# Kernel optimization log

Measured on AMD Instinct MI355X. Metric: run time of the kernel, lower is better.

The kernel has to match this reference:

```python
import jax, jax.numpy as jnp
import numpy as np

B, T, E = 4, 2048, 2048
H, KV = 16, 4
G = H // KV           # GQA group size
D = E // H            # head_dim = 128


def setup_inputs() -> dict:
    key = jax.random.key(0)
    kx, kq, kk, kv, ko = jax.random.split(key, 5)
    s = 1.0 / np.sqrt(E).astype(np.float32)
    x  = jax.random.normal(kx, (B, T, E), jnp.float32)
    Wq = jax.random.normal(kq, (E, H * D), jnp.float32) * s
    Wk = jax.random.normal(kk, (E, KV * D), jnp.float32) * s
    Wv = jax.random.normal(kv, (E, KV * D), jnp.float32) * s
    Wo = jax.random.normal(ko, (H * D, E), jnp.float32) * s
    return {"x": x, "Wq": Wq, "Wk": Wk, "Wv": Wv, "Wo": Wo}


def reference(x, Wq, Wk, Wv, Wo):
    # causal=True (default in the torch module)
    b, t, _ = x.shape
    scale = 1.0 / np.sqrt(D).astype(np.float32)
    # q heads ordered so that reshape (H,)->(KV,G) matches torch repeat_interleave
    q = (x @ Wq).reshape(b, t, KV, G, D)   # (B,T,KV,G,D)
    k = (x @ Wk).reshape(b, t, KV, D)      # (B,T,KV,D)
    v = (x @ Wv).reshape(b, t, KV, D)
    # scores per (kv-head h, group member g): (B,KV,G,T,T)
    scores = jnp.einsum('bqhgd,bkhd->bhgqk', q, k) * scale
    causal_mask = jnp.tril(jnp.ones((t, t), dtype=bool))  # True = keep
    scores = jnp.where(causal_mask, scores, -jnp.inf)
    w = jax.nn.softmax(scores, axis=-1)
    y = jnp.einsum('bhgqk,bkhd->bqhgd', w, v)  # (B,T,KV,G,D)
    y = y.reshape(b, t, H * D)
    return y @ Wo
```

## Files before the change

kernel.cpp:

```cpp
#include <hip/hip_runtime.h>

typedef unsigned short u16;
typedef __attribute__((ext_vector_type(8))) __bf16 bf16x8;
typedef __attribute__((ext_vector_type(4))) float f32x4;

#define BB 4
#define TT 2048
#define EE 2048
#define HH 16
#define KVH 4
#define DD 128

static __device__ __forceinline__ u16 f2bf(float f) {
  unsigned int u = __float_as_uint(f);
  u += 0x7fffu + ((u >> 16) & 1u);
  return (u16)(u >> 16);
}

static __device__ __forceinline__ void gl_lds16(const u16* g, u16* l) {
  __builtin_amdgcn_global_load_lds((__attribute__((address_space(1))) void*)g,
                                   (__attribute__((address_space(3))) void*)l,
                                   16, 0, 0);
}

__global__ __launch_bounds__(256) void cvt_f32_bf16(const float* __restrict__ in,
                                                    u16* __restrict__ out, int n4) {
  int i = blockIdx.x * 256 + threadIdx.x;
  if (i >= n4) return;
  float4 v = ((const float4*)in)[i];
  union { uint2 u2; u16 s[4]; } o;
  o.s[0] = f2bf(v.x); o.s[1] = f2bf(v.y); o.s[2] = f2bf(v.z); o.s[3] = f2bf(v.w);
  ((uint2*)out)[i] = o.u2;
}

__global__ __launch_bounds__(256) void transpose_w(const float* __restrict__ W,
                                                   u16* __restrict__ Wt, int R, int C) {
  __shared__ float tile[32][33];
  int tx = threadIdx.x & 31, ty = threadIdx.x >> 5;
  int r0 = blockIdx.y * 32, c0 = blockIdx.x * 32;
  #pragma unroll
  for (int i = ty; i < 32; i += 8)
    tile[i][tx] = W[(size_t)(r0 + i) * C + (c0 + tx)];
  __syncthreads();
  #pragma unroll
  for (int i = ty; i < 32; i += 8)
    Wt[(size_t)(c0 + i) * R + (r0 + tx)] = f2bf(tile[tx][i]);
}

__global__ __launch_bounds__(256) void transpose_v(const u16* __restrict__ KVb,
                                                   u16* __restrict__ VTg) {
  __shared__ u16 tile[32][36];
  const int tid = threadIdx.x;
  const int t0 = blockIdx.x * 32, d0 = blockIdx.y * 32;
  const int z = blockIdx.z;
  const int vb = z * 128;
  const size_t srcbase = (size_t)(z >> 2) * TT * 1024 + 512 + (z & 3) * 128;
  {
    int i = tid >> 3, c4 = (tid & 7) * 4;
    union { uint2 u; u16 s[4]; } r;
    r.u = *(const uint2*)(KVb + srcbase + (size_t)(t0 + i) * 1024 + d0 + c4);
    tile[i][c4] = r.s[0]; tile[i][c4 + 1] = r.s[1];
    tile[i][c4 + 2] = r.s[2]; tile[i][c4 + 3] = r.s[3];
  }
  __syncthreads();
  {
    int j = tid >> 3, cc = (tid & 7) * 4;
    union { uint2 u; u16 s[4]; } w;
    w.s[0] = tile[cc][j]; w.s[1] = tile[cc + 1][j];
    w.s[2] = tile[cc + 2][j]; w.s[3] = tile[cc + 3][j];
    *(uint2*)(VTg + (size_t)(vb + d0 + j) * TT + t0 + cc) = w.u;
  }
}

template <int MODE>
__global__ __launch_bounds__(512) void gemm256(const u16* __restrict__ A,
                                               const u16* __restrict__ Bt0,
                                               const u16* __restrict__ Bt1,
                                               void* __restrict__ C0,
                                               void* __restrict__ C1,
                                               int M, int N0, int N1, int K, int nbx) {
  __shared__ __align__(16) u16 sh[2][4][8192];
  const int tid = threadIdx.x;
  const int lane = tid & 63, wave = tid >> 6;
  const int quad = lane >> 4, n16 = lane & 15;
  const int mi = wave >> 2, ni = wave & 3;

  const int nwg = gridDim.x;
  int wg = blockIdx.x;
  wg = (wg & 7) * (nwg >> 3) + (wg >> 3);
  const int bx = wg % nbx, by = wg / nbx;
  const size_t rowbase = (size_t)by * 256;
  const int colbase = bx * 256;

  const u16* Bt = Bt0;
  int bcol = colbase;
  if (MODE == 1 && colbase >= N0) { Bt = Bt1; bcol = colbase - N0; }

  const int c0 = tid, c1 = tid + 512;
  const int r0s = c0 >> 3, ci0 = (c0 & 7) ^ (r0s & 7);
  const int r1s = c1 >> 3, ci1 = (c1 & 7) ^ (r1s & 7);
  const u16* Ag0 = A + (rowbase + r0s) * (size_t)K + ci0 * 8;
  const u16* Ag1 = A + (rowbase + r1s) * (size_t)K + ci1 * 8;
  const u16* Bg0 = Bt + ((size_t)bcol + r0s) * K + ci0 * 8;
  const u16* Bg1 = Bt + ((size_t)bcol + r1s) * K + ci1 * 8;
  const size_t h128K = (size_t)128 * K;

#define STAGE(ob, h, kb) do {                                              \
    if ((h) < 2) {                                                         \
      gl_lds16(Ag0 + (size_t)(h) * h128K + (kb), &sh[ob][h][c0 * 8]);      \
      gl_lds16(Ag1 + (size_t)(h) * h128K + (kb), &sh[ob][h][c1 * 8]);      \
    } else {                                                               \
      gl_lds16(Bg0 + (size_t)((h) - 2) * h128K + (kb), &sh[ob][h][c0 * 8]);\
      gl_lds16(Bg1 + (size_t)((h) - 2) * h128K + (kb), &sh[ob][h][c1 * 8]);\
    } } while (0)

#define LDA_HALF(mh) do {                                                  \
    _Pragma("unroll") for (int m = 0; m < 4; ++m)                          \
      _Pragma("unroll") for (int kk = 0; kk < 2; ++kk) {                   \
        int row_ = ((mh) * 4 + m) * 16 + n16;                              \
        int c_ = row_ * 8 + ((kk * 4 + quad) ^ (n16 & 7));                 \
        af[m][kk] = *(const bf16x8*)&sh[buf][mi][c_ * 8];                  \
      } } while (0)

#define LDB_HALF(nh, BF) do {                                              \
    _Pragma("unroll") for (int n = 0; n < 2; ++n)                          \
      _Pragma("unroll") for (int kk = 0; kk < 2; ++kk) {                   \
        int row_ = (ni & 1) * 64 + ((nh) * 2 + n) * 16 + n16;              \
        int c_ = row_ * 8 + ((kk * 4 + quad) ^ (n16 & 7));                 \
        BF[n][kk] = *(const bf16x8*)&sh[buf][2 + (ni >> 1)][c_ * 8];       \
      } } while (0)

#define DO_QUAD(mh, nh, BF) do {                                           \
    __builtin_amdgcn_s_setprio(1);                                         \
    _Pragma("unroll") for (int m = 0; m < 4; ++m)                          \
      _Pragma("unroll") for (int n = 0; n < 2; ++n)                        \
        _Pragma("unroll") for (int kk = 0; kk < 2; ++kk)                   \
          acc[(mh) * 4 + m][(nh) * 2 + n] =                                \
              __builtin_amdgcn_mfma_f32_16x16x32_bf16(                     \
                  af[m][kk], BF[n][kk], acc[(mh) * 4 + m][(nh) * 2 + n],   \
                  0, 0, 0);                                                \
    __builtin_amdgcn_s_setprio(0);                                         \
  } while (0)

#define FENCE() asm volatile("" ::: "memory")

  f32x4 acc[8][4];
  #pragma unroll
  for (int i = 0; i < 8; ++i)
    #pragma unroll
    for (int j = 0; j < 4; ++j) acc[i][j] = (f32x4){0.f, 0.f, 0.f, 0.f};

  bf16x8 af[4][2], bf0[2][2], bf1[2][2];
  const int nt = K / 64;

  STAGE(0, 0, 0); STAGE(0, 1, 0); STAGE(0, 2, 0); STAGE(0, 3, 0);

  #pragma unroll 2
  for (int t = 0; t < nt; ++t) {
    const int buf = t & 1, ob = buf ^ 1;
    const int kbn = (t + 1) * 64;
    const bool pre = (t + 1 < nt);

    if (pre) {
      STAGE(ob, 0, kbn);
      asm volatile("s_waitcnt vmcnt(2)" ::: "memory");
    } else {
      asm volatile("s_waitcnt vmcnt(0)" ::: "memory");
    }
    __builtin_amdgcn_s_barrier(); FENCE();
    LDA_HALF(0); LDB_HALF(0, bf0);
    DO_QUAD(0, 0, bf0);
    __builtin_amdgcn_s_barrier(); FENCE();

    LDB_HALF(1, bf1);
    if (pre) STAGE(ob, 1, kbn);
    __builtin_amdgcn_s_barrier(); FENCE();
    DO_QUAD(0, 1, bf1);
    __builtin_amdgcn_s_barrier(); FENCE();

    LDA_HALF(1);
    if (pre) STAGE(ob, 2, kbn);
    __builtin_amdgcn_s_barrier(); FENCE();
    DO_QUAD(1, 1, bf1);
    __builtin_amdgcn_s_barrier(); FENCE();

    if (pre) STAGE(ob, 3, kbn);
    __builtin_amdgcn_s_barrier(); FENCE();
    DO_QUAD(1, 0, bf0);
    __builtin_amdgcn_s_barrier(); FENCE();
  }

#undef STAGE
#undef LDA_HALF
#undef LDB_HALF
#undef DO_QUAD
#undef FENCE

  const size_t crow0 = rowbase + (size_t)mi * 128;
  #pragma unroll
  for (int mt = 0; mt < 8; ++mt) {
    #pragma unroll
    for (int r = 0; r < 4; ++r) {
      size_t row = crow0 + mt * 16 + quad * 4 + r;
      #pragma unroll
      for (int nt_ = 0; nt_ < 4; ++nt_) {
        int col = colbase + ni * 64 + nt_ * 16 + n16;
        float v = acc[mt][nt_][r];
        if (MODE == 0) {
          ((float*)C0)[row * (size_t)N0 + col] = v;
        } else {
          if (col < N0) ((u16*)C0)[row * (size_t)N0 + col] = f2bf(v);
          else          ((u16*)C1)[row * (size_t)N1 + (col - N0)] = f2bf(v);
        }
      }
    }
  }
}

__global__ __launch_bounds__(256) void attn_kernel(const u16* __restrict__ Qm,
                                                   const u16* __restrict__ KVm,
                                                   const u16* __restrict__ VTg,
                                                   u16* __restrict__ Ym) {
  __shared__ u16 Ks[32 * 128];
  __shared__ u16 Vt[128 * 32];
  __shared__ u16 Pb[4 * 32 * 40];

  const int tid = threadIdx.x;
  const int lane = tid & 63, wave = tid >> 6;
  const int quad = lane >> 4, n16 = lane & 15;
  const int b = blockIdx.y >> 4, h = blockIdx.y & 15;
  const int kvh = h >> 2;
  const int kvbase = b * TT;
  const u16* VTg_ = VTg + (size_t)((b * 4 + kvh) * 128) * TT;

  const int krow = tid >> 4;
  const int kslot = tid & 15;
  const int kg = (kslot ^ krow) * 8;
  u16* Ksd0 = &Ks[krow * 128 + kslot * 8];
  u16* Ksd1 = &Ks[(krow + 16) * 128 + kslot * 8];
  const int vrow = tid >> 2, vc = (tid & 3) * 8;
  u16* Vtd0 = &Vt[vrow * 32 + vc];
  u16* Vtd1 = &Vt[(vrow + 64) * 32 + vc];

  constexpr float SCL = 0.08838834764831843f * 1.4426950408889634f;

  for (int pass = 0; pass < 2; ++pass) {
    const int qt = pass ? 15 - (int)blockIdx.x : (int)blockIdx.x;
    const int q0 = qt * 128;
    const size_t qrowbase = (size_t)(b * TT + q0);
    const int wq0 = wave * 32;

    bf16x8 aq[2][4];
    #pragma unroll
    for (int mt = 0; mt < 2; ++mt) {
      const u16* qp = Qm + (qrowbase + wq0 + mt * 16 + n16) * (HH * DD) + h * DD + quad * 8;
      #pragma unroll
      for (int dt = 0; dt < 4; ++dt)
        aq[mt][dt] = *(const bf16x8*)(qp + dt * 32);
    }

    float lrow[2][4];
    f32x4 oacc[2][8];
    #pragma unroll
    for (int mt = 0; mt < 2; ++mt) {
      #pragma unroll
      for (int r = 0; r < 4; ++r) lrow[mt][r] = 0.f;
      #pragma unroll
      for (int i = 0; i < 8; ++i) oacc[mt][i] = (f32x4){0.f, 0.f, 0.f, 0.f};
    }

    const int kend = q0 + 128;
    for (int kb = 0; kb < kend; kb += 32) {
      __syncthreads();
      gl_lds16(KVm + (size_t)(kvbase + kb + krow) * 1024 + kvh * DD + kg, Ksd0);
      gl_lds16(KVm + (size_t)(kvbase + kb + krow + 16) * 1024 + kvh * DD + kg, Ksd1);
      gl_lds16(VTg_ + (size_t)vrow * TT + kb + vc, Vtd0);
      gl_lds16(VTg_ + (size_t)(vrow + 64) * TT + kb + vc, Vtd1);
      __syncthreads();

      f32x4 sf[2][2];
      #pragma unroll
      for (int half = 0; half < 2; ++half) {
        bf16x8 bk[4];
        #pragma unroll
        for (int dt = 0; dt < 4; ++dt) {
          int slot = (dt * 4 + quad) ^ n16;
          bk[dt] = *(const bf16x8*)&Ks[(half * 16 + n16) * 128 + slot * 8];
        }
        #pragma unroll
        for (int mt = 0; mt < 2; ++mt) {
          f32x4 s = (f32x4){0.f, 0.f, 0.f, 0.f};
          #pragma unroll
          for (int dt = 0; dt < 4; ++dt)
            s = __builtin_amdgcn_mfma_f32_16x16x32_bf16(aq[mt][dt], bk[dt], s, 0, 0, 0);
          sf[mt][half] = s;
        }
      }

      u16* pw = &Pb[wave * (32 * 40)];
      #pragma unroll
      for (int mt = 0; mt < 2; ++mt)
        #pragma unroll
        for (int half = 0; half < 2; ++half) {
          int key = kb + half * 16 + n16;
          #pragma unroll
          for (int r = 0; r < 4; ++r) {
            int qpos = q0 + wq0 + mt * 16 + quad * 4 + r;
            float pv = (key <= qpos) ? exp2f(sf[mt][half][r] * SCL) : 0.f;
            lrow[mt][r] += pv;
            pw[(mt * 16 + quad * 4 + r) * 40 + half * 16 + n16] = f2bf(pv);
          }
        }
      __builtin_amdgcn_s_waitcnt(0);
      bf16x8 ap[2];
      ap[0] = *(const bf16x8*)&pw[n16 * 40 + quad * 8];
      ap[1] = *(const bf16x8*)&pw[(16 + n16) * 40 + quad * 8];

      #pragma unroll
      for (int dt = 0; dt < 8; ++dt) {
        bf16x8 bv = *(const bf16x8*)&Vt[(dt * 16 + n16) * 32 + quad * 8];
        oacc[0][dt] = __builtin_amdgcn_mfma_f32_16x16x32_bf16(ap[0], bv, oacc[0][dt], 0, 0, 0);
        oacc[1][dt] = __builtin_amdgcn_mfma_f32_16x16x32_bf16(ap[1], bv, oacc[1][dt], 0, 0, 0);
      }
    }

    float rinv[2][4];
    #pragma unroll
    for (int mt = 0; mt < 2; ++mt)
      #pragma unroll
      for (int r = 0; r < 4; ++r) {
        float v = lrow[mt][r];
        v += __shfl_xor(v, 1, 64);
        v += __shfl_xor(v, 2, 64);
        v += __shfl_xor(v, 4, 64);
        v += __shfl_xor(v, 8, 64);
        rinv[mt][r] = 1.0f / v;
      }
    #pragma unroll
    for (int mt = 0; mt < 2; ++mt)
      #pragma unroll
      for (int dt = 0; dt < 8; ++dt)
        #pragma unroll
        for (int r = 0; r < 4; ++r) {
          size_t row = qrowbase + wq0 + mt * 16 + quad * 4 + r;
          Ym[row * (HH * DD) + h * DD + dt * 16 + n16] = f2bf(oacc[mt][dt][r] * rinv[mt][r]);
        }
  }
}

extern "C" void kernel_launch(void* const* d_in, const int* in_sizes, int n_in,
                              void* d_out, int out_size, void* d_ws, size_t ws_size,
                              hipStream_t stream) {
  const float* x  = (const float*)d_in[0];
  const float* Wq = (const float*)d_in[1];
  const float* Wk = (const float*)d_in[2];
  const float* Wv = (const float*)d_in[3];
  const float* Wo = (const float*)d_in[4];
  float* out = (float*)d_out;

  u16* ws   = (u16*)d_ws;
  u16* xb   = ws;
  u16* Wbuf = xb + (size_t)8192 * 2048;
  u16* Yb   = xb;

  u16* ob   = (u16*)d_out;
  u16* Qb   = ob;
  u16* KVb  = ob + (size_t)8192 * 2048;
  u16* VTg  = ob + (size_t)8192 * 2048 + (size_t)8192 * 1024;
  u16* WkvT = VTg + (size_t)16 * 128 * 2048;

  cvt_f32_bf16<<<16384, 256, 0, stream>>>(x, xb, (4 * 2048 * 2048) / 4);

  transpose_w<<<dim3(64, 64), 256, 0, stream>>>(Wq, Wbuf, 2048, 2048);
  transpose_w<<<dim3(16, 64), 256, 0, stream>>>(Wk, WkvT, 2048, 512);
  transpose_w<<<dim3(16, 64), 256, 0, stream>>>(Wv, WkvT + (size_t)512 * 2048, 2048, 512);

  gemm256<1><<<384, 512, 0, stream>>>(xb, Wbuf, WkvT, (void*)Qb, (void*)KVb,
                                      8192, 2048, 1024, 2048, 12);

  transpose_v<<<dim3(64, 4, 16), 256, 0, stream>>>(KVb, VTg);

  attn_kernel<<<dim3(8, 64), 256, 0, stream>>>(Qb, KVb, VTg, Yb);

  transpose_w<<<dim3(64, 64), 256, 0, stream>>>(Wo, Wbuf, 2048, 2048);
  gemm256<0><<<256, 512, 0, stream>>>(Yb, Wbuf, nullptr, (void*)out, nullptr,
                                      8192, 2048, 0, 2048, 8);
}
```

Measured before the change: 477.4 us.

## Double-buffer K/V staging in attention, one q-tile per block, skip masked tiles

The attention kernel now double-buffers its K and V tiles in LDS, prefetching the next key block with async global-to-LDS loads while the current one is computed, and waits on the vmcnt counter instead of a pair of __syncthreads. The two-pass work balancing (pairing tile i with 15-i) is replaced by a grid of 16 q-tiles with the heaviest tiles first. Waves skip key blocks that lie fully beyond their causal window, apply the mask only on diagonal blocks, pack probabilities with v_cvt_pk_bf16_f32, swizzle the V tile layout against bank conflicts, and raise wave priority around MFMA sections. This trades more LDS per block and a less even per-block workload for overlap of loads with compute and less masking and conversion work.

```diff
diff --git a/kernel.cpp b/kernel.cpp
--- a/kernel.cpp
+++ b/kernel.cpp
@@ -221,8 +221,8 @@
                                                    const u16* __restrict__ KVm,
                                                    const u16* __restrict__ VTg,
                                                    u16* __restrict__ Ym) {
-  __shared__ u16 Ks[32 * 128];
-  __shared__ u16 Vt[128 * 32];
+  __shared__ u16 Ks[2][32 * 128];
+  __shared__ u16 Vt[2][128 * 32];
   __shared__ u16 Pb[4 * 32 * 40];
 
   const int tid = threadIdx.x;
@@ -233,51 +233,63 @@
   const int kvbase = b * TT;
   const u16* VTg_ = VTg + (size_t)((b * 4 + kvh) * 128) * TT;
 
-  const int krow = tid >> 4;
-  const int kslot = tid & 15;
+  const int krow = tid >> 4, kslot = tid & 15;
   const int kg = (kslot ^ krow) * 8;
-  u16* Ksd0 = &Ks[krow * 128 + kslot * 8];
-  u16* Ksd1 = &Ks[(krow + 16) * 128 + kslot * 8];
-  const int vrow = tid >> 2, vc = (tid & 3) * 8;
-  u16* Vtd0 = &Vt[vrow * 32 + vc];
-  u16* Vtd1 = &Vt[(vrow + 64) * 32 + vc];
+  const int vrow = tid >> 2, vs = tid & 3;
+  const int vq8 = (vs ^ ((tid >> 3) & 3)) * 8;
+
+#define STAGEKV(bi, kb) do {                                                          \
+    gl_lds16(KVm + (size_t)(kvbase + (kb) + krow) * 1024 + kvh * DD + kg,             \
+             &Ks[bi][krow * 128 + kslot * 8]);                                        \
+    gl_lds16(KVm + (size_t)(kvbase + (kb) + krow + 16) * 1024 + kvh * DD + kg,        \
+             &Ks[bi][(krow + 16) * 128 + kslot * 8]);                                 \
+    gl_lds16(VTg_ + (size_t)vrow * TT + (kb) + vq8, &Vt[bi][vrow * 32 + vs * 8]);     \
+    gl_lds16(VTg_ + (size_t)(vrow + 64) * TT + (kb) + vq8,                            \
+             &Vt[bi][(vrow + 64) * 32 + vs * 8]);                                     \
+  } while (0)
 
   constexpr float SCL = 0.08838834764831843f * 1.4426950408889634f;
 
-  for (int pass = 0; pass < 2; ++pass) {
-    const int qt = pass ? 15 - (int)blockIdx.x : (int)blockIdx.x;
-    const int q0 = qt * 128;
-    const size_t qrowbase = (size_t)(b * TT + q0);
-    const int wq0 = wave * 32;
-
-    bf16x8 aq[2][4];
-    #pragma unroll
-    for (int mt = 0; mt < 2; ++mt) {
-      const u16* qp = Qm + (qrowbase + wq0 + mt * 16 + n16) * (HH * DD) + h * DD + quad * 8;
-      #pragma unroll
-      for (int dt = 0; dt < 4; ++dt)
-        aq[mt][dt] = *(const bf16x8*)(qp + dt * 32);
+  const int qt = 15 - (int)blockIdx.x;
+  const int q0 = qt * 128;
+  const size_t qrowbase = (size_t)(b * TT + q0);
+  const int wq0 = wave * 32;
+  const int qmin = q0 + wq0;
+
+  bf16x8 aq[2][4];
+  #pragma unroll
+  for (int mt = 0; mt < 2; ++mt) {
+    const u16* qp = Qm + (qrowbase + wq0 + mt * 16 + n16) * (HH * DD) + h * DD + quad * 8;
+    #pragma unroll
+    for (int dt = 0; dt < 4; ++dt)
+      aq[mt][dt] = *(const bf16x8*)(qp + dt * 32);
+  }
+
+  float lrow[2][4];
+  f32x4 oacc[2][8];
+  #pragma unroll
+  for (int mt = 0; mt < 2; ++mt) {
+    #pragma unroll
+    for (int r = 0; r < 4; ++r) lrow[mt][r] = 0.f;
+    #pragma unroll
+    for (int i = 0; i < 8; ++i) oacc[mt][i] = (f32x4){0.f, 0.f, 0.f, 0.f};
+  }
+
+  const int kend = q0 + 128;
+  STAGEKV(0, 0);
+  for (int kb = 0; kb < kend; kb += 32) {
+    const int bi = (kb >> 5) & 1;
+    const bool pre = (kb + 32 < kend);
+    if (pre) {
+      STAGEKV(bi ^ 1, kb + 32);
+      asm volatile("s_waitcnt vmcnt(4)" ::: "memory");
+    } else {
+      asm volatile("s_waitcnt vmcnt(0)" ::: "memory");
     }
-
-    float lrow[2][4];
-    f32x4 oacc[2][8];
-    #pragma unroll
-    for (int mt = 0; mt < 2; ++mt) {
-      #pragma unroll
-      for (int r = 0; r < 4; ++r) lrow[mt][r] = 0.f;
-      #pragma unroll
-      for (int i = 0; i < 8; ++i) oacc[mt][i] = (f32x4){0.f, 0.f, 0.f, 0.f};
-    }
-
-    const int kend = q0 + 128;
-    for (int kb = 0; kb < kend; kb += 32) {
-      __syncthreads();
-      gl_lds16(KVm + (size_t)(kvbase + kb + krow) * 1024 + kvh * DD + kg, Ksd0);
-      gl_lds16(KVm + (size_t)(kvbase + kb + krow + 16) * 1024 + kvh * DD + kg, Ksd1);
-      gl_lds16(VTg_ + (size_t)vrow * TT + kb + vc, Vtd0);
-      gl_lds16(VTg_ + (size_t)(vrow + 64) * TT + kb + vc, Vtd1);
-      __syncthreads();
-
+    __builtin_amdgcn_s_barrier();
+    asm volatile("" ::: "memory");
+
+    if (kb <= qmin + 31) {
       f32x4 sf[2][2];
       #pragma unroll
       for (int half = 0; half < 2; ++half) {
@@ -285,8 +297,9 @@
         #pragma unroll
         for (int dt = 0; dt < 4; ++dt) {
           int slot = (dt * 4 + quad) ^ n16;
-          bk[dt] = *(const bf16x8*)&Ks[(half * 16 + n16) * 128 + slot * 8];
+          bk[dt] = *(const bf16x8*)&Ks[bi][(half * 16 + n16) * 128 + slot * 8];
         }
+        __builtin_amdgcn_s_setprio(1);
         #pragma unroll
         for (int mt = 0; mt < 2; ++mt) {
           f32x4 s = (f32x4){0.f, 0.f, 0.f, 0.f};
@@ -295,57 +308,82 @@
             s = __builtin_amdgcn_mfma_f32_16x16x32_bf16(aq[mt][dt], bk[dt], s, 0, 0, 0);
           sf[mt][half] = s;
         }
+        __builtin_amdgcn_s_setprio(0);
       }
 
       u16* pw = &Pb[wave * (32 * 40)];
+      const bool needmask = (kb + 31 > qmin);
       #pragma unroll
-      for (int mt = 0; mt < 2; ++mt)
+      for (int mt = 0; mt < 2; ++mt) {
         #pragma unroll
         for (int half = 0; half < 2; ++half) {
-          int key = kb + half * 16 + n16;
-          #pragma unroll
-          for (int r = 0; r < 4; ++r) {
-            int qpos = q0 + wq0 + mt * 16 + quad * 4 + r;
-            float pv = (key <= qpos) ? exp2f(sf[mt][half][r] * SCL) : 0.f;
-            lrow[mt][r] += pv;
-            pw[(mt * 16 + quad * 4 + r) * 40 + half * 16 + n16] = f2bf(pv);
+          const int key = kb + half * 16 + n16;
+          float p0 = exp2f(sf[mt][half][0] * SCL);
+          float p1 = exp2f(sf[mt][half][1] * SCL);
+          float p2 = exp2f(sf[mt][half][2] * SCL);
+          float p3 = exp2f(sf[mt][half][3] * SCL);
+          if (needmask) {
+            const int qp0 = qmin + mt * 16 + quad * 4;
+            if (key > qp0)     p0 = 0.f;
+            if (key > qp0 + 1) p1 = 0.f;
+            if (key > qp0 + 2) p2 = 0.f;
+            if (key > qp0 + 3) p3 = 0.f;
           }
+          lrow[mt][0] += p0; lrow[mt][1] += p1;
+          lrow[mt][2] += p2; lrow[mt][3] += p3;
+          unsigned pk01, pk23;
+          asm("v_cvt_pk_bf16_f32 %0, %1, %2" : "=v"(pk01) : "v"(p0), "v"(p1));
+          asm("v_cvt_pk_bf16_f32 %0, %1, %2" : "=v"(pk23) : "v"(p2), "v"(p3));
+          const int pb = (mt * 16 + quad * 4) * 40 + half * 16 + n16;
+          pw[pb]       = (u16)pk01;
+          pw[pb + 40]  = (u16)(pk01 >> 16);
+          pw[pb + 80]  = (u16)pk23;
+          pw[pb + 120] = (u16)(pk23 >> 16);
         }
-      __builtin_amdgcn_s_waitcnt(0);
-      bf16x8 ap[2];
-      ap[0] = *(const bf16x8*)&pw[n16 * 40 + quad * 8];
-      ap[1] = *(const bf16x8*)&pw[(16 + n16) * 40 + quad * 8];
-
+      }
+      asm volatile("s_waitcnt lgkmcnt(0)" ::: "memory");
+      __builtin_amdgcn_sched_barrier(0);
+      bf16x8 ap0 = *(const bf16x8*)&pw[n16 * 40 + quad * 8];
+      bf16x8 ap1 = *(const bf16x8*)&pw[(16 + n16) * 40 + quad * 8];
+
+      __builtin_amdgcn_s_setprio(1);
       #pragma unroll
       for (int dt = 0; dt < 8; ++dt) {
-        bf16x8 bv = *(const bf16x8*)&Vt[(dt * 16 + n16) * 32 + quad * 8];
-        oacc[0][dt] = __builtin_amdgcn_mfma_f32_16x16x32_bf16(ap[0], bv, oacc[0][dt], 0, 0, 0);
-        oacc[1][dt] = __builtin_amdgcn_mfma_f32_16x16x32_bf16(ap[1], bv, oacc[1][dt], 0, 0, 0);
+        bf16x8 bv = *(const bf16x8*)&Vt[bi][(dt * 16 + n16) * 32 +
+                                           ((quad ^ ((n16 >> 1) & 3)) * 8)];
+        oacc[0][dt] = __builtin_amdgcn_mfma_f32_16x16x32_bf16(ap0, bv, oacc[0][dt], 0, 0, 0);
+        oacc[1][dt] = __builtin_amdgcn_mfma_f32_16x16x32_bf16(ap1, bv, oacc[1][dt], 0, 0, 0);
       }
+      __builtin_amdgcn_s_setprio(0);
     }
 
-    float rinv[2][4];
-    #pragma unroll
-    for (int mt = 0; mt < 2; ++mt)
+    asm volatile("" ::: "memory");
+    __builtin_amdgcn_s_barrier();
+    asm volatile("" ::: "memory");
+  }
+
+  float rinv[2][4];
+  #pragma unroll
+  for (int mt = 0; mt < 2; ++mt)
+    #pragma unroll
+    for (int r = 0; r < 4; ++r) {
+      float v = lrow[mt][r];
+      v += __shfl_xor(v, 1, 64);
+      v += __shfl_xor(v, 2, 64);
+      v += __shfl_xor(v, 4, 64);
+      v += __shfl_xor(v, 8, 64);
+      rinv[mt][r] = 1.0f / v;
+    }
+  #pragma unroll
+  for (int mt = 0; mt < 2; ++mt)
+    #pragma unroll
+    for (int dt = 0; dt < 8; ++dt)
       #pragma unroll
       for (int r = 0; r < 4; ++r) {
-        float v = lrow[mt][r];
-        v += __shfl_xor(v, 1, 64);
-        v += __shfl_xor(v, 2, 64);
-        v += __shfl_xor(v, 4, 64);
-        v += __shfl_xor(v, 8, 64);
-        rinv[mt][r] = 1.0f / v;
+        size_t row = qrowbase + wq0 + mt * 16 + quad * 4 + r;
+        Ym[row * (HH * DD) + h * DD + dt * 16 + n16] = f2bf(oacc[mt][dt][r] * rinv[mt][r]);
       }
-    #pragma unroll
-    for (int mt = 0; mt < 2; ++mt)
-      #pragma unroll
-      for (int dt = 0; dt < 8; ++dt)
-        #pragma unroll
-        for (int r = 0; r < 4; ++r) {
-          size_t row = qrowbase + wq0 + mt * 16 + quad * 4 + r;
-          Ym[row * (HH * DD) + h * DD + dt * 16 + n16] = f2bf(oacc[mt][dt][r] * rinv[mt][r]);
-        }
-  }
+#undef STAGEKV
 }
 
 extern "C" void kernel_launch(void* const* d_in, const int* in_sizes, int n_in,
@@ -380,7 +418,7 @@
 
   transpose_v<<<dim3(64, 4, 16), 256, 0, stream>>>(KVb, VTg);
 
-  attn_kernel<<<dim3(8, 64), 256, 0, stream>>>(Qb, KVb, VTg, Yb);
+  attn_kernel<<<dim3(16, 64), 256, 0, stream>>>(Qb, KVb, VTg, Yb);
 
   transpose_w<<<dim3(64, 64), 256, 0, stream>>>(Wo, Wbuf, 2048, 2048);
   gemm256<0><<<256, 512, 0, stream>>>(Yb, Wbuf, nullptr, (void*)out, nullptr,
```

Measured after the change: 578.8 us. 1.21x slower.
